# Performance work log

Hardware: AMD Instinct MI355X
Metric: run time of the kernel (lower is better)

Reference implementation:

```python
import jax, jax.numpy as jnp
import numpy as np

IGNORE_INDEX = -100


def setup_inputs() -> dict:
    key = jax.random.key(0)
    k_e, k_c, k_t = jax.random.split(key, 3)
    B, T, D, V = 1, 8192, 1024, 50257
    e = jax.random.normal(k_e, (B, T, D), dtype=jnp.float32)
    c = jax.random.normal(k_c, (V, D), dtype=jnp.float32) * (D ** -0.5)
    targets = jax.random.randint(k_t, (B, T), 0, V, dtype=jnp.int64)
    bias = jnp.zeros((V,), dtype=jnp.float32)
    return {"e": e, "c": c, "targets": targets, "bias": bias}


def _linear_cross_entropy(e, c, bias, targets, ignore_index=IGNORE_INDEX,
                          softcap=None, reduction="mean"):
    B, T, D = e.shape
    V = c.shape[0]
    ef = e.reshape(B * T, D)
    tf = targets.reshape(B * T)
    # logits: [N, V] = e @ c^T + bias
    logits = jnp.einsum("nd,vd->nv", ef, c) + bias
    if softcap is not None:
        logits = softcap * jnp.tanh(logits / softcap)
    # stable cross entropy: lse - logit[target]
    lse = jax.nn.logsumexp(logits, axis=-1)  # [N]
    safe_t = jnp.where(tf == ignore_index, 0, tf)
    tgt_logit = jnp.take_along_axis(logits, safe_t[:, None], axis=-1)[:, 0]
    nll = lse - tgt_logit  # [N]
    valid = (tf != ignore_index)
    nll = jnp.where(valid, nll, 0.0)
    if reduction == "mean":
        denom = jnp.maximum(valid.sum().astype(nll.dtype), 1.0)
        return nll.sum() / denom
    elif reduction == "sum":
        return nll.sum()
    else:  # 'none'
        return nll.reshape(B, T)


def reference(e, c, targets, bias):
    return _linear_cross_entropy(e, c, bias, targets)
```

## Files before the change

### kernel.cpp

```cpp
#include <hip/hip_runtime.h>
#include <hip/hip_bf16.h>
#include <math.h>


#define BM 128
#define BN 128
#define BKB 128

typedef int   i32x8 __attribute__((ext_vector_type(8)));
typedef float f32x4 __attribute__((ext_vector_type(4)));

__device__ __forceinline__ void load_lds16(const void* g, void* l) {
    __builtin_amdgcn_global_load_lds(
        (const __attribute__((address_space(1))) void*)g,
        (__attribute__((address_space(3))) void*)l, 16, 0, 0);
}

__device__ __forceinline__ unsigned char f2e4m3_sw(float x) {
    unsigned u = __float_as_uint(x);
    unsigned s = (u >> 24) & 0x80;
    float ax = __uint_as_float(u & 0x7fffffff);
    if (ax != ax) return (unsigned char)(s | 0x7f);
    if (ax >= 448.f) return (unsigned char)(s | 0x7e);
    if (ax < 0.0009765625f) return (unsigned char)s;
    if (ax < 0.015625f) {
        int n = (int)rintf(ax * 512.f);
        return (unsigned char)(s | n);
    }
    int e = (int)((u >> 23) & 0xff) - 127;
    unsigned m = u & 0x7fffff;
    unsigned keep = m >> 20, rest = m & 0xfffff;
    if (rest > 0x80000u || (rest == 0x80000u && (keep & 1))) keep++;
    if (keep == 8) { keep = 0; e++; if (e > 8) return (unsigned char)(s | 0x7e); }
    return (unsigned char)(s | ((e + 7) << 3) | keep);
}

__device__ __forceinline__ unsigned int pk4_fp8(float a, float b, float c, float d) {
#if __has_builtin(__builtin_amdgcn_cvt_pk_fp8_f32)
    int v = __builtin_amdgcn_cvt_pk_fp8_f32(a, b, 0, false);
    v = __builtin_amdgcn_cvt_pk_fp8_f32(c, d, v, true);
    return (unsigned int)v;
#else
    return (unsigned int)f2e4m3_sw(a) | ((unsigned int)f2e4m3_sw(b) << 8) |
           ((unsigned int)f2e4m3_sw(c) << 16) | ((unsigned int)f2e4m3_sw(d) << 24);
#endif
}

__global__ void cast_f32_fp8(const float* __restrict__ src,
                             unsigned int* __restrict__ dst,
                             long n_src, long n_dst, float scale) {
    long i8 = ((long)blockIdx.x * blockDim.x + threadIdx.x) * 8;
    if (i8 >= n_dst) return;
    uint2 o;
    if (i8 + 7 < n_src) {
        float4 v0 = *(const float4*)(src + i8);
        float4 v1 = *(const float4*)(src + i8 + 4);
        o.x = pk4_fp8(v0.x * scale, v0.y * scale, v0.z * scale, v0.w * scale);
        o.y = pk4_fp8(v1.x * scale, v1.y * scale, v1.z * scale, v1.w * scale);
    } else {
        o.x = o.y = 0u;
    }
    *(uint2*)((unsigned char*)dst + i8) = o;
}

__global__ __launch_bounds__(256)
void gemm_lse_partial(const unsigned char* __restrict__ E,
                      const unsigned char* __restrict__ C,
                      const float* __restrict__ bias,
                      float* __restrict__ ps,
                      int N, int D, int V) {
    __shared__ unsigned char As[BM * BKB];
    __shared__ unsigned char Bs[BN * BKB];
    __shared__ float bias_s[BN];
    __shared__ float red_s[2][BM];

    const int t = threadIdx.x;
    const int w = t >> 6;
    const int l = t & 63;
    const int quad = l >> 4;
    const int lm = l & 15;
    const int wr0 = (w >> 1) * 64;
    const int wc0 = (w & 1) * 64;

    const int mt = blockIdx.x;
    const int vt = blockIdx.y;

    if (t < BN) {
        int col = vt * BN + t;
        bias_s[t] = (col < V) ? bias[col] : -INFINITY;
    }

    const int srow = t >> 3;
    const int schunk = (t & 7) ^ (srow & 7);
    const unsigned char* ga = E + (long)(mt * BM + srow) * D + schunk * 16;
    const unsigned char* gb = C + (long)(vt * BN + srow) * D + schunk * 16;
    char* lA = (char*)As + w * 1024;
    char* lB = (char*)Bs + w * 1024;
    const long rnd = 32L * D;

    f32x4 acc[4][4] = {};
    const int sA = 127;
    const int sB = 123;

    for (int k0 = 0; k0 < D; k0 += BKB) {
#pragma unroll
        for (int ro = 0; ro < 4; ro++) {
            load_lds16(ga + k0 + ro * rnd, lA + ro * 4096);
            load_lds16(gb + k0 + ro * rnd, lB + ro * 4096);
        }
        __syncthreads();

        const int c0 = ((quad << 1) ^ (lm & 7)) << 4;
        const int c1 = c0 ^ 16;
        i32x8 a_frag[4], b_frag[4];
#pragma unroll
        for (int ti = 0; ti < 4; ti++) {
            const unsigned char* pr = As + (wr0 + ti * 16 + lm) * 128;
            int4 lo = *(const int4*)(pr + c0);
            int4 hi = *(const int4*)(pr + c1);
            a_frag[ti] = (i32x8){lo.x, lo.y, lo.z, lo.w, hi.x, hi.y, hi.z, hi.w};
        }
#pragma unroll
        for (int tj = 0; tj < 4; tj++) {
            const unsigned char* pr = Bs + (wc0 + tj * 16 + lm) * 128;
            int4 lo = *(const int4*)(pr + c0);
            int4 hi = *(const int4*)(pr + c1);
            b_frag[tj] = (i32x8){lo.x, lo.y, lo.z, lo.w, hi.x, hi.y, hi.z, hi.w};
        }
#pragma unroll
        for (int ti = 0; ti < 4; ti++)
#pragma unroll
            for (int tj = 0; tj < 4; tj++)
                acc[ti][tj] = __builtin_amdgcn_mfma_scale_f32_16x16x128_f8f6f4(
                    a_frag[ti], b_frag[tj], acc[ti][tj], 0, 0, 0, sA, 0, sB);
        __syncthreads();
    }

    float bvals[4];
#pragma unroll
    for (int tj = 0; tj < 4; tj++) bvals[tj] = bias_s[wc0 + tj * 16 + lm];

#pragma unroll
    for (int ti = 0; ti < 4; ti++) {
#pragma unroll
        for (int r = 0; r < 4; r++) {
            float srow_ = 0.f;
#pragma unroll
            for (int tj = 0; tj < 4; tj++)
                srow_ += __expf(acc[ti][tj][r] + bvals[tj]);
#pragma unroll
            for (int off = 1; off < 16; off <<= 1)
                srow_ += __shfl_xor(srow_, off, 64);
            if (lm == 0)
                red_s[w & 1][wr0 + ti * 16 + quad * 4 + r] = srow_;
        }
    }
    __syncthreads();
    if (t < BM) {
        long grow = (long)mt * BM + t;
        ps[(long)vt * N + grow] = red_s[0][t] + red_s[1][t];
    }
}

__global__ void tgt_logit_kernel(const float* __restrict__ E,
                                 const float* __restrict__ C,
                                 const float* __restrict__ bias,
                                 const int* __restrict__ targets,
                                 float* __restrict__ tgt, int N, int D) {
    int row = blockIdx.x * 4 + (threadIdx.x >> 6);
    int l = threadIdx.x & 63;
    if (row >= N) return;
    int tg = targets[row];
    int tt = (tg < 0) ? 0 : tg;
    const float4* e4 = (const float4*)(E + (long)row * D);
    const float4* c4 = (const float4*)(C + (long)tt * D);
    float acc = 0.f;
    for (int j = l; j < D / 4; j += 64) {
        float4 a = e4[j], b = c4[j];
        acc += a.x * b.x + a.y * b.y + a.z * b.z + a.w * b.w;
    }
#pragma unroll
    for (int off = 32; off; off >>= 1) acc += __shfl_xor(acc, off, 64);
    if (l == 0) tgt[row] = acc + bias[tt];
}

__global__ void lse_part(const float* __restrict__ ps,
                         float* __restrict__ part,
                         int N, int vtiles, int chunk) {
    int r = blockIdx.x * 256 + threadIdx.x;
    int p = blockIdx.y;
    if (r >= N) return;
    int v0 = p * chunk, v1 = min(v0 + chunk, vtiles);
    float s = 0.f;
    for (int vt = v0; vt < v1; vt++) s += ps[(long)vt * N + r];
    part[(long)p * N + r] = s;
}

__global__ void lse_finish(const float* __restrict__ part,
                           const float* __restrict__ tgt,
                           const int* __restrict__ targets,
                           float* __restrict__ gacc, int N, int P) {
    __shared__ float sred[8];
    int r = blockIdx.x * 256 + threadIdx.x;
    float nll = 0.f, cnt = 0.f;
    if (r < N) {
        float s = 0.f;
        for (int p = 0; p < P; p++) s += part[(long)p * N + r];
        int tg = targets[r];
        if (tg != -100) { nll = logf(s) - tgt[r]; cnt = 1.f; }
    }
#pragma unroll
    for (int off = 32; off; off >>= 1) {
        nll += __shfl_xor(nll, off, 64);
        cnt += __shfl_xor(cnt, off, 64);
    }
    int w = threadIdx.x >> 6, l = threadIdx.x & 63;
    if (l == 0) { sred[w] = nll; sred[4 + w] = cnt; }
    __syncthreads();
    if (threadIdx.x == 0) {
        float S = sred[0] + sred[1] + sred[2] + sred[3];
        float C = sred[4] + sred[5] + sred[6] + sred[7];
        atomicAdd(gacc, S);
        atomicAdd(gacc + 1, C);
    }
}

__global__ void final_scalar(const float* __restrict__ gacc, float* __restrict__ out) {
    out[0] = gacc[0] / fmaxf(gacc[1], 1.f);
}

extern "C" void kernel_launch(void* const* d_in, const int* in_sizes, int n_in,
                              void* d_out, int out_size, void* d_ws, size_t ws_size,
                              hipStream_t stream) {
    const float* e       = (const float*)d_in[0];
    const float* c       = (const float*)d_in[1];
    const int*   targets = (const int*)d_in[2];
    const float* bias    = (const float*)d_in[3];
    float* out = (float*)d_out;

    const int N = in_sizes[2];
    const int V = in_sizes[3];
    const int D = in_sizes[0] / N;
    const int mtiles = N / BM;
    const int vtiles = (V + BN - 1) / BN;
    const long Vpad = (long)vtiles * BN;
    const int P = 8;
    const int chunk = (vtiles + P - 1) / P;

    char* ws = (char*)d_ws;
    size_t off = 0;
    auto alloc = [&](size_t bytes) {
        void* p = ws + off;
        off += (bytes + 255) & ~(size_t)255;
        return p;
    };
    unsigned char* e_f8 = (unsigned char*)alloc((size_t)N * D);
    unsigned char* c_f8 = (unsigned char*)alloc((size_t)Vpad * D);
    float* ps   = (float*)alloc((size_t)vtiles * N * 4);
    float* tgt  = (float*)alloc((size_t)N * 4);
    float* part = (float*)alloc((size_t)P * N * 4);
    float* gacc = (float*)alloc(8);

    hipMemsetAsync(gacc, 0, 8, stream);

    const long ne = (long)N * D;
    const long ncs = (long)V * D;
    const long ncd = Vpad * D;
    cast_f32_fp8<<<(int)((ne / 8 + 255) / 256), 256, 0, stream>>>(
        e, (unsigned int*)e_f8, ne, ne, 1.0f);
    cast_f32_fp8<<<(int)((ncd / 8 + 255) / 256), 256, 0, stream>>>(
        c, (unsigned int*)c_f8, ncs, ncd, 16.0f);

    dim3 grid(mtiles, vtiles);
    gemm_lse_partial<<<grid, 256, 0, stream>>>(e_f8, c_f8, bias, ps, N, D, V);

    tgt_logit_kernel<<<N / 4, 256, 0, stream>>>(e, c, bias, targets, tgt, N, D);
    lse_part<<<dim3(N / 256, P), 256, 0, stream>>>(ps, part, N, vtiles, chunk);
    lse_finish<<<N / 256, 256, 0, stream>>>(part, tgt, targets, gacc, N, P);
    final_scalar<<<1, 1, 0, stream>>>(gacc, out);
}
```

Measured before the change: 859.4 us.

## Fuse target-logit extraction and row-sum reduction into the FP8 GEMM epilogue

The GEMM epilogue now captures the target logit directly from the accumulator tile and atomically adds per-tile exp sums into a per-row buffer. This removes the separate fp32 target-logit kernel, the large partial-sum buffer, and the two-stage reduction kernels. The two cast kernels are also merged into one launch. In exchange there are many float atomics per row across v-tiles, and the target logit now comes from FP8-quantized values with C scaled by 16, which may change accuracy and the scaling of the captured logit.

```diff
diff --git a/kernel.cpp b/kernel.cpp
--- a/kernel.cpp
+++ b/kernel.cpp
@@ -46,32 +46,49 @@
 #endif
 }
 
-__global__ void cast_f32_fp8(const float* __restrict__ src,
-                             unsigned int* __restrict__ dst,
-                             long n_src, long n_dst, float scale) {
+__global__ void cast_all_fp8(const float* __restrict__ e,
+                             const float* __restrict__ c,
+                             unsigned char* __restrict__ e_f8,
+                             unsigned char* __restrict__ c_f8,
+                             long ne, long ncs, long ncd) {
     long i8 = ((long)blockIdx.x * blockDim.x + threadIdx.x) * 8;
-    if (i8 >= n_dst) return;
+    if (i8 >= ne + ncd) return;
+    const float* src;
+    unsigned char* dst;
+    float scale;
+    bool zero = false;
+    if (i8 < ne) {
+        src = e + i8; dst = e_f8 + i8; scale = 1.0f;
+    } else {
+        long j8 = i8 - ne;
+        dst = c_f8 + j8; scale = 16.0f;
+        src = c + j8;
+        zero = (j8 + 7 >= ncs);
+    }
     uint2 o;
-    if (i8 + 7 < n_src) {
-        float4 v0 = *(const float4*)(src + i8);
-        float4 v1 = *(const float4*)(src + i8 + 4);
+    if (!zero) {
+        float4 v0 = *(const float4*)(src);
+        float4 v1 = *(const float4*)(src + 4);
         o.x = pk4_fp8(v0.x * scale, v0.y * scale, v0.z * scale, v0.w * scale);
         o.y = pk4_fp8(v1.x * scale, v1.y * scale, v1.z * scale, v1.w * scale);
     } else {
         o.x = o.y = 0u;
     }
-    *(uint2*)((unsigned char*)dst + i8) = o;
+    *(uint2*)dst = o;
 }
 
 __global__ __launch_bounds__(256)
 void gemm_lse_partial(const unsigned char* __restrict__ E,
                       const unsigned char* __restrict__ C,
                       const float* __restrict__ bias,
-                      float* __restrict__ ps,
+                      const int* __restrict__ targets,
+                      float* __restrict__ row_sum,
+                      float* __restrict__ tgt,
                       int N, int D, int V) {
     __shared__ unsigned char As[BM * BKB];
     __shared__ unsigned char Bs[BN * BKB];
     __shared__ float bias_s[BN];
+    __shared__ int tgt_s[BM];
     __shared__ float red_s[2][BM];
 
     const int t = threadIdx.x;
@@ -89,6 +106,8 @@
         int col = vt * BN + t;
         bias_s[t] = (col < V) ? bias[col] : -INFINITY;
     }
+    if (t >= BN && t < BN + BM)
+        tgt_s[t - BN] = targets[mt * BM + (t - BN)];
 
     const int srow = t >> 3;
     const int schunk = (t & 7) ^ (srow & 7);
@@ -144,70 +163,38 @@
     for (int ti = 0; ti < 4; ti++) {
 #pragma unroll
         for (int r = 0; r < 4; r++) {
+            const int row_local = wr0 + ti * 16 + quad * 4 + r;
+            const int tl = tgt_s[row_local] - vt * BN;
             float srow_ = 0.f;
 #pragma unroll
-            for (int tj = 0; tj < 4; tj++)
-                srow_ += __expf(acc[ti][tj][r] + bvals[tj]);
+            for (int tj = 0; tj < 4; tj++) {
+                float v = acc[ti][tj][r] + bvals[tj];
+                srow_ += __expf(v);
+                if (wc0 + tj * 16 + lm == tl)
+                    tgt[mt * BM + row_local] = v;
+            }
 #pragma unroll
             for (int off = 1; off < 16; off <<= 1)
                 srow_ += __shfl_xor(srow_, off, 64);
             if (lm == 0)
-                red_s[w & 1][wr0 + ti * 16 + quad * 4 + r] = srow_;
+                red_s[w & 1][row_local] = srow_;
         }
     }
     __syncthreads();
-    if (t < BM) {
-        long grow = (long)mt * BM + t;
-        ps[(long)vt * N + grow] = red_s[0][t] + red_s[1][t];
-    }
-}
-
-__global__ void tgt_logit_kernel(const float* __restrict__ E,
-                                 const float* __restrict__ C,
-                                 const float* __restrict__ bias,
-                                 const int* __restrict__ targets,
-                                 float* __restrict__ tgt, int N, int D) {
-    int row = blockIdx.x * 4 + (threadIdx.x >> 6);
-    int l = threadIdx.x & 63;
-    if (row >= N) return;
-    int tg = targets[row];
-    int tt = (tg < 0) ? 0 : tg;
-    const float4* e4 = (const float4*)(E + (long)row * D);
-    const float4* c4 = (const float4*)(C + (long)tt * D);
-    float acc = 0.f;
-    for (int j = l; j < D / 4; j += 64) {
-        float4 a = e4[j], b = c4[j];
-        acc += a.x * b.x + a.y * b.y + a.z * b.z + a.w * b.w;
-    }
-#pragma unroll
-    for (int off = 32; off; off >>= 1) acc += __shfl_xor(acc, off, 64);
-    if (l == 0) tgt[row] = acc + bias[tt];
-}
-
-__global__ void lse_part(const float* __restrict__ ps,
-                         float* __restrict__ part,
-                         int N, int vtiles, int chunk) {
-    int r = blockIdx.x * 256 + threadIdx.x;
-    int p = blockIdx.y;
-    if (r >= N) return;
-    int v0 = p * chunk, v1 = min(v0 + chunk, vtiles);
-    float s = 0.f;
-    for (int vt = v0; vt < v1; vt++) s += ps[(long)vt * N + r];
-    part[(long)p * N + r] = s;
-}
-
-__global__ void lse_finish(const float* __restrict__ part,
+    if (t < BM)
+        atomicAdd(&row_sum[(long)mt * BM + t], red_s[0][t] + red_s[1][t]);
+}
+
+__global__ void lse_finish(const float* __restrict__ row_sum,
                            const float* __restrict__ tgt,
                            const int* __restrict__ targets,
-                           float* __restrict__ gacc, int N, int P) {
+                           float* __restrict__ gacc, int N) {
     __shared__ float sred[8];
     int r = blockIdx.x * 256 + threadIdx.x;
     float nll = 0.f, cnt = 0.f;
     if (r < N) {
-        float s = 0.f;
-        for (int p = 0; p < P; p++) s += part[(long)p * N + r];
         int tg = targets[r];
-        if (tg != -100) { nll = logf(s) - tgt[r]; cnt = 1.f; }
+        if (tg != -100) { nll = logf(row_sum[r]) - tgt[r]; cnt = 1.f; }
     }
 #pragma unroll
     for (int off = 32; off; off >>= 1) {
@@ -218,10 +205,8 @@
     if (l == 0) { sred[w] = nll; sred[4 + w] = cnt; }
     __syncthreads();
     if (threadIdx.x == 0) {
-        float S = sred[0] + sred[1] + sred[2] + sred[3];
-        float C = sred[4] + sred[5] + sred[6] + sred[7];
-        atomicAdd(gacc, S);
-        atomicAdd(gacc + 1, C);
+        atomicAdd(gacc, sred[0] + sred[1] + sred[2] + sred[3]);
+        atomicAdd(gacc + 1, sred[4] + sred[5] + sred[6] + sred[7]);
     }
 }
 
@@ -244,8 +229,6 @@
     const int mtiles = N / BM;
     const int vtiles = (V + BN - 1) / BN;
     const long Vpad = (long)vtiles * BN;
-    const int P = 8;
-    const int chunk = (vtiles + P - 1) / P;
 
     char* ws = (char*)d_ws;
     size_t off = 0;
@@ -256,26 +239,23 @@
     };
     unsigned char* e_f8 = (unsigned char*)alloc((size_t)N * D);
     unsigned char* c_f8 = (unsigned char*)alloc((size_t)Vpad * D);
-    float* ps   = (float*)alloc((size_t)vtiles * N * 4);
-    float* tgt  = (float*)alloc((size_t)N * 4);
-    float* part = (float*)alloc((size_t)P * N * 4);
-    float* gacc = (float*)alloc(8);
-
-    hipMemsetAsync(gacc, 0, 8, stream);
-
-    const long ne = (long)N * D;
+    float* row_sum = (float*)alloc((size_t)N * 4);
+    float* gacc    = (float*)alloc(8);
+    float* tgt     = (float*)alloc((size_t)N * 4);
+
+    hipMemsetAsync(row_sum, 0, (size_t)N * 4 + 256 + 8, stream);
+
+    const long ne  = (long)N * D;
     const long ncs = (long)V * D;
     const long ncd = Vpad * D;
-    cast_f32_fp8<<<(int)((ne / 8 + 255) / 256), 256, 0, stream>>>(
-        e, (unsigned int*)e_f8, ne, ne, 1.0f);
-    cast_f32_fp8<<<(int)((ncd / 8 + 255) / 256), 256, 0, stream>>>(
-        c, (unsigned int*)c_f8, ncs, ncd, 16.0f);
+    const long tot8 = (ne + ncd) / 8;
+    cast_all_fp8<<<(int)((tot8 + 255) / 256), 256, 0, stream>>>(
+        e, c, e_f8, c_f8, ne, ncs, ncd);
 
     dim3 grid(mtiles, vtiles);
-    gemm_lse_partial<<<grid, 256, 0, stream>>>(e_f8, c_f8, bias, ps, N, D, V);
-
-    tgt_logit_kernel<<<N / 4, 256, 0, stream>>>(e, c, bias, targets, tgt, N, D);
-    lse_part<<<dim3(N / 256, P), 256, 0, stream>>>(ps, part, N, vtiles, chunk);
-    lse_finish<<<N / 256, 256, 0, stream>>>(part, tgt, targets, gacc, N, P);
+    gemm_lse_partial<<<grid, 256, 0, stream>>>(e_f8, c_f8, bias, targets,
+                                               row_sum, tgt, N, D, V);
+
+    lse_finish<<<(N + 255) / 256, 256, 0, stream>>>(row_sum, tgt, targets, gacc, N);
     final_scalar<<<1, 1, 0, stream>>>(gacc, out);
 }
```

After: 821.7 us. -4.4%, faster.
